# Kernel tuning notes

Hardware: AMD Instinct MI355X
Metric: run time of the kernel (lower is better)

## Reference

```python
import jax, jax.numpy as jnp
import numpy as np

N = 50000   # nodes
E = 800000  # edges (avg degree 16)
D = 96      # input feature dim
U = 96      # units (== D, so no dense_i projection)


def _glorot(key, fan_in, fan_out):
    limit = np.sqrt(6.0 / (fan_in + fan_out)).astype(np.float32)
    return jax.random.uniform(key, (fan_in, fan_out), jnp.float32, -limit, limit)


def setup_inputs() -> dict:
    key = jax.random.key(0)
    ks = jax.random.split(key, 8)
    X = jax.random.normal(ks[0], (N, D), jnp.float32)
    row = jax.random.randint(ks[1], (E,), 0, N, jnp.int32)   # destination nodes
    col = jax.random.randint(ks[2], (E,), 0, N, jnp.int32)   # source nodes
    a_vals = jax.random.uniform(ks[3], (E,), jnp.float32)    # adjacency values
    return {
        "X": X,
        "a_vals": a_vals,
        "Wn": _glorot(ks[4], D, U), "bn": jnp.zeros((U,), jnp.float32),
        "Wgi": _glorot(ks[5], D, U), "bgi": jnp.zeros((U,), jnp.float32),
        "Wgn": _glorot(ks[6], U, U), "bgn": jnp.zeros((U,), jnp.float32),
        "row": row, "col": col,
    }


def reference(X, a_vals, Wn, bn, Wgi, bgi, Wgn, bgn, row, col):
    # new_X = dense_n(X); new_X = A @ new_X  (SpMM via gather + segment_sum)
    newX = X @ Wn + bn                       # [N, U]
    msgs = a_vals[:, None] * newX[col]       # [E, U]
    agg = jax.ops.segment_sum(msgs, row, num_segments=N)  # [N, U]
    # gate = sigmoid(dense_gate_i(X) + dense_gate_n(agg))
    gate = jax.nn.sigmoid(X @ Wgi + bgi + agg @ Wgn + bgn)
    # units == inp_dim -> no dense_i; gated residual combine
    return agg * gate + X * (1.0 - gate)
```

## Files before the change

kernel.cpp:

```cpp
#include <hip/hip_runtime.h>
#include <math.h>


#define DU 96
#define DU4 24
#define NCH 12
#define CAP 32

typedef unsigned int uint;
typedef unsigned short ushort;
typedef __attribute__((ext_vector_type(8))) short short8;
typedef __attribute__((ext_vector_type(4))) float f32x4;

__device__ inline uint bf16r(float x) {
  uint u = __float_as_uint(x);
  return (u + 0x7FFFu + ((u >> 16) & 1u)) >> 16;
}

__global__ __launch_bounds__(256) void k_fuse1(
    const float* __restrict__ X, const float* __restrict__ Wn,
    const float* __restrict__ bn, const float* __restrict__ Wgi,
    const float* __restrict__ Wgn, const int* __restrict__ row,
    const int* __restrict__ col, const float* __restrict__ a_vals,
    ushort* __restrict__ Xb, ushort* __restrict__ newXb,
    ushort* __restrict__ WTgi, ushort* __restrict__ WTgn,
    int* __restrict__ cnt8, int2* __restrict__ epad8, int N, int E, int ntile) {
  __shared__ ushort WL[9216];
  __shared__ ushort Xs[64][104];
  const int tid = threadIdx.x;
  const int lane = tid & 63, w = tid >> 6;
  const int m = lane & 15, q = lane >> 4;

  if ((int)blockIdx.x < ntile) {
    if (blockIdx.x == 0) {
      for (int i = tid; i < DU * DU; i += 256) {
        int n = i / DU, k = i % DU;
        WTgi[i] = (ushort)bf16r(Wgi[k * DU + n]);
      }
    } else if (blockIdx.x == 1) {
      for (int i = tid; i < DU * DU; i += 256) {
        int n = i / DU, k = i % DU;
        WTgn[i] = (ushort)bf16r(Wgn[k * DU + n]);
      }
    }
    for (int idx = tid; idx < 9216; idx += 256) {
      int j = idx & 7, ln = (idx >> 3) & 63, tk = idx >> 9;
      int ks = tk / 6, t = tk % 6;
      int k = ks * 32 + (ln >> 4) * 8 + j;
      int n = t * 16 + (ln & 15);
      WL[idx] = (ushort)bf16r(Wn[k * DU + n]);
    }
    const int row0 = blockIdx.x * 64;
    for (int i = tid; i < 64 * 48; i += 256) {
      int r = i / 48, cu = i % 48;
      int gr = row0 + r;
      uint packed = 0;
      if (gr < N) {
        float2 v = ((const float2*)X)[(size_t)gr * 48 + cu];
        packed = bf16r(v.x) | (bf16r(v.y) << 16);
        ((uint*)Xb)[(size_t)gr * 48 + cu] = packed;
      }
      *(uint*)&Xs[r][cu * 2] = packed;
    }
    __syncthreads();

    f32x4 acc[6];
#pragma unroll
    for (int t = 0; t < 6; ++t) acc[t] = (f32x4){0.f, 0.f, 0.f, 0.f};
#pragma unroll
    for (int ks = 0; ks < 3; ++ks) {
      short8 af = *(const short8*)&Xs[w * 16 + m][ks * 32 + q * 8];
#pragma unroll
      for (int t = 0; t < 6; ++t) {
        short8 bf = *(const short8*)&WL[((ks * 6 + t) * 64 + lane) * 8];
        acc[t] = __builtin_amdgcn_mfma_f32_16x16x32_bf16(af, bf, acc[t], 0, 0, 0);
      }
    }
    __syncthreads();
#pragma unroll
    for (int t = 0; t < 6; ++t) {
      int c = t * 16 + m;
      float bb = bn[c];
#pragma unroll
      for (int i = 0; i < 4; ++i)
        Xs[w * 16 + q * 4 + i][c] = (ushort)bf16r(acc[t][i] + bb);
    }
    __syncthreads();
    for (int i = tid; i < 64 * 48; i += 256) {
      int r = i / 48, cu = i % 48;
      int gr = row0 + r;
      if (gr < N) ((uint*)newXb)[(size_t)gr * 48 + cu] = *(uint*)&Xs[r][cu * 2];
    }
  }

  {
    const int g = blockIdx.x & 7;
    int* cnt = cnt8 + (size_t)g * N;
    int2* ep = epad8 + (size_t)g * N * CAP;
    for (int i = blockIdx.x * 256 + tid; i < E; i += gridDim.x * 256) {
      int d = row[i];
      int slot = atomicAdd(&cnt[d], 1);
      if (slot < CAP)
        ep[(size_t)d * CAP + slot] = make_int2(col[i], __float_as_int(a_vals[i]));
    }
  }
}

__global__ __launch_bounds__(256) void k_agg(const ushort* __restrict__ newXb,
                                             const int* __restrict__ cnt8,
                                             const int2* __restrict__ epad8,
                                             ushort* __restrict__ aggb, int N) {
  int i = blockIdx.x * 256 + threadIdx.x;
  int r = i / NCH;
  int c = i % NCH;
  if (r >= N) return;
  float acc[8];
#pragma unroll
  for (int j = 0; j < 8; ++j) acc[j] = 0.f;

#pragma unroll
  for (int g = 0; g < 8; ++g) {
    int e1 = cnt8[(size_t)g * N + r];
    if (e1 > CAP) e1 = CAP;
    const int2* ep = epad8 + ((size_t)g * N + r) * CAP;
    int e = 0;
    for (; e + 2 <= e1; e += 2) {
      int2 p0 = ep[e + 0];
      int2 p1 = ep[e + 1];
      uint4 v0 = *(const uint4*)(newXb + (size_t)p0.x * DU + c * 8);
      uint4 v1 = *(const uint4*)(newXb + (size_t)p1.x * DU + c * 8);
      float a0 = __int_as_float(p0.y), a1 = __int_as_float(p1.y);
      acc[0] = fmaf(a0, __uint_as_float(v0.x << 16), acc[0]);
      acc[1] = fmaf(a0, __uint_as_float(v0.x & 0xFFFF0000u), acc[1]);
      acc[2] = fmaf(a0, __uint_as_float(v0.y << 16), acc[2]);
      acc[3] = fmaf(a0, __uint_as_float(v0.y & 0xFFFF0000u), acc[3]);
      acc[4] = fmaf(a0, __uint_as_float(v0.z << 16), acc[4]);
      acc[5] = fmaf(a0, __uint_as_float(v0.z & 0xFFFF0000u), acc[5]);
      acc[6] = fmaf(a0, __uint_as_float(v0.w << 16), acc[6]);
      acc[7] = fmaf(a0, __uint_as_float(v0.w & 0xFFFF0000u), acc[7]);
      acc[0] = fmaf(a1, __uint_as_float(v1.x << 16), acc[0]);
      acc[1] = fmaf(a1, __uint_as_float(v1.x & 0xFFFF0000u), acc[1]);
      acc[2] = fmaf(a1, __uint_as_float(v1.y << 16), acc[2]);
      acc[3] = fmaf(a1, __uint_as_float(v1.y & 0xFFFF0000u), acc[3]);
      acc[4] = fmaf(a1, __uint_as_float(v1.z << 16), acc[4]);
      acc[5] = fmaf(a1, __uint_as_float(v1.z & 0xFFFF0000u), acc[5]);
      acc[6] = fmaf(a1, __uint_as_float(v1.w << 16), acc[6]);
      acc[7] = fmaf(a1, __uint_as_float(v1.w & 0xFFFF0000u), acc[7]);
    }
    if (e < e1) {
      int2 p = ep[e];
      uint4 v = *(const uint4*)(newXb + (size_t)p.x * DU + c * 8);
      float a = __int_as_float(p.y);
      acc[0] = fmaf(a, __uint_as_float(v.x << 16), acc[0]);
      acc[1] = fmaf(a, __uint_as_float(v.x & 0xFFFF0000u), acc[1]);
      acc[2] = fmaf(a, __uint_as_float(v.y << 16), acc[2]);
      acc[3] = fmaf(a, __uint_as_float(v.y & 0xFFFF0000u), acc[3]);
      acc[4] = fmaf(a, __uint_as_float(v.z << 16), acc[4]);
      acc[5] = fmaf(a, __uint_as_float(v.z & 0xFFFF0000u), acc[5]);
      acc[6] = fmaf(a, __uint_as_float(v.w << 16), acc[6]);
      acc[7] = fmaf(a, __uint_as_float(v.w & 0xFFFF0000u), acc[7]);
    }
  }
  uint4 o;
  o.x = bf16r(acc[0]) | (bf16r(acc[1]) << 16);
  o.y = bf16r(acc[2]) | (bf16r(acc[3]) << 16);
  o.z = bf16r(acc[4]) | (bf16r(acc[5]) << 16);
  o.w = bf16r(acc[6]) | (bf16r(acc[7]) << 16);
  *(uint4*)(aggb + (size_t)r * DU + c * 8) = o;
}

__global__ __launch_bounds__(256) void k_gateM(const ushort* __restrict__ Xb,
                                               const ushort* __restrict__ aggb,
                                               const ushort* __restrict__ WTgi,
                                               const ushort* __restrict__ WTgn,
                                               const float* __restrict__ bgi,
                                               const float* __restrict__ bgn,
                                               const float* __restrict__ X,
                                               float* __restrict__ Out, int N) {
  __shared__ float Gs[64][100];
  const int tid = threadIdx.x;
  const int lane = tid & 63, w = tid >> 6;
  const int m = lane & 15, q = lane >> 4;
  const int row0 = blockIdx.x * 64;
  int ar = row0 + w * 16 + m;
  if (ar > N - 1) ar = N - 1;

  f32x4 acc[6];
#pragma unroll
  for (int t = 0; t < 6; ++t) acc[t] = (f32x4){0.f, 0.f, 0.f, 0.f};

#pragma unroll
  for (int ks = 0; ks < 3; ++ks) {
    short8 af = *(const short8*)(Xb + (size_t)ar * DU + ks * 32 + q * 8);
#pragma unroll
    for (int t = 0; t < 6; ++t) {
      short8 bf = *(const short8*)(WTgi + (size_t)(t * 16 + m) * DU + ks * 32 + q * 8);
      acc[t] = __builtin_amdgcn_mfma_f32_16x16x32_bf16(af, bf, acc[t], 0, 0, 0);
    }
  }
#pragma unroll
  for (int ks = 0; ks < 3; ++ks) {
    short8 af = *(const short8*)(aggb + (size_t)ar * DU + ks * 32 + q * 8);
#pragma unroll
    for (int t = 0; t < 6; ++t) {
      short8 bf = *(const short8*)(WTgn + (size_t)(t * 16 + m) * DU + ks * 32 + q * 8);
      acc[t] = __builtin_amdgcn_mfma_f32_16x16x32_bf16(af, bf, acc[t], 0, 0, 0);
    }
  }

#pragma unroll
  for (int t = 0; t < 6; ++t) {
    int c = t * 16 + m;
    float bb = bgi[c] + bgn[c];
#pragma unroll
    for (int i = 0; i < 4; ++i) {
      float z = acc[t][i] + bb;
      Gs[w * 16 + q * 4 + i][c] = 1.f / (1.f + __expf(-z));
    }
  }
  __syncthreads();

  for (int j = tid; j < 64 * DU4; j += 256) {
    int r = j / DU4, c = j % DU4;
    int gr = row0 + r;
    if (gr < N) {
      float4 xv = ((const float4*)X)[(size_t)gr * DU4 + c];
      uint2 av = ((const uint2*)aggb)[(size_t)gr * DU4 + c];
      float a0 = __uint_as_float(av.x << 16);
      float a1 = __uint_as_float(av.x & 0xFFFF0000u);
      float a2 = __uint_as_float(av.y << 16);
      float a3 = __uint_as_float(av.y & 0xFFFF0000u);
      const float* gp = &Gs[r][c * 4];
      float4 o;
      o.x = xv.x + gp[0] * (a0 - xv.x);
      o.y = xv.y + gp[1] * (a1 - xv.y);
      o.z = xv.z + gp[2] * (a2 - xv.z);
      o.w = xv.w + gp[3] * (a3 - xv.w);
      ((float4*)Out)[(size_t)gr * DU4 + c] = o;
    }
  }
}

extern "C" void kernel_launch(void* const* d_in, const int* in_sizes, int n_in,
                              void* d_out, int out_size, void* d_ws, size_t ws_size,
                              hipStream_t stream) {
  const float* X      = (const float*)d_in[0];
  const float* a_vals = (const float*)d_in[1];
  const float* Wn     = (const float*)d_in[2];
  const float* bn     = (const float*)d_in[3];
  const float* Wgi    = (const float*)d_in[4];
  const float* bgi    = (const float*)d_in[5];
  const float* Wgn    = (const float*)d_in[6];
  const float* bgn    = (const float*)d_in[7];
  const int*   row    = (const int*)d_in[8];
  const int*   col    = (const int*)d_in[9];
  float* out = (float*)d_out;

  const int N = in_sizes[0] / DU;
  const int E = in_sizes[1];
  const int ntile = (N + 63) / 64;
  const int G1 = ((ntile + 7) / 8) * 8;

  int2*   epad8 = (int2*)d_ws;
  ushort* Xb    = (ushort*)(epad8 + (size_t)8 * N * CAP);
  ushort* newXb = Xb + (size_t)N * DU;
  ushort* aggb  = newXb + (size_t)N * DU;
  ushort* WTgi  = aggb + (size_t)N * DU;
  ushort* WTgn  = WTgi + DU * DU;
  int*    cnt8  = (int*)(WTgn + DU * DU);

  hipMemsetAsync(cnt8, 0, (size_t)8 * N * sizeof(int), stream);

  k_fuse1<<<G1, 256, 0, stream>>>(X, Wn, bn, Wgi, Wgn, row, col, a_vals,
                                  Xb, newXb, WTgi, WTgn, cnt8, epad8, N, E, ntile);
  k_agg  <<<((size_t)N * NCH + 255) / 256, 256, 0, stream>>>(newXb, cnt8, epad8, aggb, N);
  k_gateM<<<ntile, 256, 0, stream>>>(Xb, aggb, WTgi, WTgn, bgi, bgn, X, out, N);
}
```

Before: 224.4 us.

## Fuse SpMM aggregation into gate kernel and interleave per-node edge buckets

Merges the aggregation kernel into the gate/MFMA kernel so aggregated rows stay in shared memory rather than going through a global bf16 buffer, which removes one launch and the aggb write and reread. The edge padding layout changes from eight separate per-group arrays (cap 32 each) to one interleaved 128-slot region per node (cap 16 per group), giving better locality for a node's edges. The fused kernel uses 512 threads and splits the MFMA columns across wave pairs. The risks are less parallelism during the gather phase, since each block only has 768 work items, and dropped edges if a node gets more than 16 edges from one group.

```diff
diff --git a/kernel.cpp b/kernel.cpp
--- a/kernel.cpp
+++ b/kernel.cpp
@@ -4,8 +4,7 @@
 
 #define DU 96
 #define DU4 24
-#define NCH 12
-#define CAP 32
+#define CAPG 16
 
 typedef unsigned int uint;
 typedef unsigned short ushort;
@@ -24,7 +23,7 @@
     const int* __restrict__ col, const float* __restrict__ a_vals,
     ushort* __restrict__ Xb, ushort* __restrict__ newXb,
     ushort* __restrict__ WTgi, ushort* __restrict__ WTgn,
-    int* __restrict__ cnt8, int2* __restrict__ epad8, int N, int E, int ntile) {
+    int* __restrict__ cnt8, int2* __restrict__ epad, int N, int E, int ntile) {
   __shared__ ushort WL[9216];
   __shared__ ushort Xs[64][104];
   const int tid = threadIdx.x;
@@ -96,136 +95,141 @@
   {
     const int g = blockIdx.x & 7;
     int* cnt = cnt8 + (size_t)g * N;
-    int2* ep = epad8 + (size_t)g * N * CAP;
     for (int i = blockIdx.x * 256 + tid; i < E; i += gridDim.x * 256) {
       int d = row[i];
       int slot = atomicAdd(&cnt[d], 1);
-      if (slot < CAP)
-        ep[(size_t)d * CAP + slot] = make_int2(col[i], __float_as_int(a_vals[i]));
-    }
-  }
-}
-
-__global__ __launch_bounds__(256) void k_agg(const ushort* __restrict__ newXb,
-                                             const int* __restrict__ cnt8,
-                                             const int2* __restrict__ epad8,
-                                             ushort* __restrict__ aggb, int N) {
-  int i = blockIdx.x * 256 + threadIdx.x;
-  int r = i / NCH;
-  int c = i % NCH;
-  if (r >= N) return;
-  float acc[8];
-#pragma unroll
-  for (int j = 0; j < 8; ++j) acc[j] = 0.f;
-
-#pragma unroll
-  for (int g = 0; g < 8; ++g) {
-    int e1 = cnt8[(size_t)g * N + r];
-    if (e1 > CAP) e1 = CAP;
-    const int2* ep = epad8 + ((size_t)g * N + r) * CAP;
-    int e = 0;
-    for (; e + 2 <= e1; e += 2) {
-      int2 p0 = ep[e + 0];
-      int2 p1 = ep[e + 1];
-      uint4 v0 = *(const uint4*)(newXb + (size_t)p0.x * DU + c * 8);
-      uint4 v1 = *(const uint4*)(newXb + (size_t)p1.x * DU + c * 8);
-      float a0 = __int_as_float(p0.y), a1 = __int_as_float(p1.y);
-      acc[0] = fmaf(a0, __uint_as_float(v0.x << 16), acc[0]);
-      acc[1] = fmaf(a0, __uint_as_float(v0.x & 0xFFFF0000u), acc[1]);
-      acc[2] = fmaf(a0, __uint_as_float(v0.y << 16), acc[2]);
-      acc[3] = fmaf(a0, __uint_as_float(v0.y & 0xFFFF0000u), acc[3]);
-      acc[4] = fmaf(a0, __uint_as_float(v0.z << 16), acc[4]);
-      acc[5] = fmaf(a0, __uint_as_float(v0.z & 0xFFFF0000u), acc[5]);
-      acc[6] = fmaf(a0, __uint_as_float(v0.w << 16), acc[6]);
-      acc[7] = fmaf(a0, __uint_as_float(v0.w & 0xFFFF0000u), acc[7]);
-      acc[0] = fmaf(a1, __uint_as_float(v1.x << 16), acc[0]);
-      acc[1] = fmaf(a1, __uint_as_float(v1.x & 0xFFFF0000u), acc[1]);
-      acc[2] = fmaf(a1, __uint_as_float(v1.y << 16), acc[2]);
-      acc[3] = fmaf(a1, __uint_as_float(v1.y & 0xFFFF0000u), acc[3]);
-      acc[4] = fmaf(a1, __uint_as_float(v1.z << 16), acc[4]);
-      acc[5] = fmaf(a1, __uint_as_float(v1.z & 0xFFFF0000u), acc[5]);
-      acc[6] = fmaf(a1, __uint_as_float(v1.w << 16), acc[6]);
-      acc[7] = fmaf(a1, __uint_as_float(v1.w & 0xFFFF0000u), acc[7]);
-    }
-    if (e < e1) {
-      int2 p = ep[e];
-      uint4 v = *(const uint4*)(newXb + (size_t)p.x * DU + c * 8);
-      float a = __int_as_float(p.y);
-      acc[0] = fmaf(a, __uint_as_float(v.x << 16), acc[0]);
-      acc[1] = fmaf(a, __uint_as_float(v.x & 0xFFFF0000u), acc[1]);
-      acc[2] = fmaf(a, __uint_as_float(v.y << 16), acc[2]);
-      acc[3] = fmaf(a, __uint_as_float(v.y & 0xFFFF0000u), acc[3]);
-      acc[4] = fmaf(a, __uint_as_float(v.z << 16), acc[4]);
-      acc[5] = fmaf(a, __uint_as_float(v.z & 0xFFFF0000u), acc[5]);
-      acc[6] = fmaf(a, __uint_as_float(v.w << 16), acc[6]);
-      acc[7] = fmaf(a, __uint_as_float(v.w & 0xFFFF0000u), acc[7]);
-    }
-  }
-  uint4 o;
-  o.x = bf16r(acc[0]) | (bf16r(acc[1]) << 16);
-  o.y = bf16r(acc[2]) | (bf16r(acc[3]) << 16);
-  o.z = bf16r(acc[4]) | (bf16r(acc[5]) << 16);
-  o.w = bf16r(acc[6]) | (bf16r(acc[7]) << 16);
-  *(uint4*)(aggb + (size_t)r * DU + c * 8) = o;
-}
-
-__global__ __launch_bounds__(256) void k_gateM(const ushort* __restrict__ Xb,
-                                               const ushort* __restrict__ aggb,
-                                               const ushort* __restrict__ WTgi,
-                                               const ushort* __restrict__ WTgn,
-                                               const float* __restrict__ bgi,
-                                               const float* __restrict__ bgn,
-                                               const float* __restrict__ X,
-                                               float* __restrict__ Out, int N) {
+      if (slot < CAPG)
+        epad[(size_t)d * 128 + g * CAPG + slot] =
+            make_int2(col[i], __float_as_int(a_vals[i]));
+    }
+  }
+}
+
+__global__ __launch_bounds__(512) void k_aggGate(
+    const ushort* __restrict__ Xb, const ushort* __restrict__ newXb,
+    const int* __restrict__ cnt8, const int2* __restrict__ epad,
+    const ushort* __restrict__ WTgi, const ushort* __restrict__ WTgn,
+    const float* __restrict__ bgi, const float* __restrict__ bgn,
+    const float* __restrict__ X, float* __restrict__ Out, int N) {
+  __shared__ ushort As[64][104];
   __shared__ float Gs[64][100];
   const int tid = threadIdx.x;
-  const int lane = tid & 63, w = tid >> 6;
+  const int lane = tid & 63;
   const int m = lane & 15, q = lane >> 4;
   const int row0 = blockIdx.x * 64;
-  int ar = row0 + w * 16 + m;
-  if (ar > N - 1) ar = N - 1;
-
-  f32x4 acc[6];
-#pragma unroll
-  for (int t = 0; t < 6; ++t) acc[t] = (f32x4){0.f, 0.f, 0.f, 0.f};
-
-#pragma unroll
-  for (int ks = 0; ks < 3; ++ks) {
-    short8 af = *(const short8*)(Xb + (size_t)ar * DU + ks * 32 + q * 8);
-#pragma unroll
-    for (int t = 0; t < 6; ++t) {
-      short8 bf = *(const short8*)(WTgi + (size_t)(t * 16 + m) * DU + ks * 32 + q * 8);
-      acc[t] = __builtin_amdgcn_mfma_f32_16x16x32_bf16(af, bf, acc[t], 0, 0, 0);
-    }
-  }
-#pragma unroll
-  for (int ks = 0; ks < 3; ++ks) {
-    short8 af = *(const short8*)(aggb + (size_t)ar * DU + ks * 32 + q * 8);
-#pragma unroll
-    for (int t = 0; t < 6; ++t) {
-      short8 bf = *(const short8*)(WTgn + (size_t)(t * 16 + m) * DU + ks * 32 + q * 8);
-      acc[t] = __builtin_amdgcn_mfma_f32_16x16x32_bf16(af, bf, acc[t], 0, 0, 0);
-    }
-  }
-
-#pragma unroll
-  for (int t = 0; t < 6; ++t) {
-    int c = t * 16 + m;
-    float bb = bgi[c] + bgn[c];
-#pragma unroll
-    for (int i = 0; i < 4; ++i) {
-      float z = acc[t][i] + bb;
-      Gs[w * 16 + q * 4 + i][c] = 1.f / (1.f + __expf(-z));
-    }
+
+  for (int j = tid; j < 64 * 12; j += 512) {
+    int lr = j / 12, c = j % 12;
+    int r = row0 + lr;
+    float acc[8];
+#pragma unroll
+    for (int k = 0; k < 8; ++k) acc[k] = 0.f;
+    if (r < N) {
+      const int2* epr = epad + (size_t)r * 128;
+#pragma unroll
+      for (int g = 0; g < 8; ++g) {
+        int e1 = cnt8[(size_t)g * N + r];
+        if (e1 > CAPG) e1 = CAPG;
+        const int2* ep = epr + g * CAPG;
+        int e = 0;
+        for (; e + 2 <= e1; e += 2) {
+          int2 p0 = ep[e + 0];
+          int2 p1 = ep[e + 1];
+          uint4 v0 = *(const uint4*)(newXb + (size_t)p0.x * DU + c * 8);
+          uint4 v1 = *(const uint4*)(newXb + (size_t)p1.x * DU + c * 8);
+          float a0 = __int_as_float(p0.y), a1 = __int_as_float(p1.y);
+          acc[0] = fmaf(a0, __uint_as_float(v0.x << 16), acc[0]);
+          acc[1] = fmaf(a0, __uint_as_float(v0.x & 0xFFFF0000u), acc[1]);
+          acc[2] = fmaf(a0, __uint_as_float(v0.y << 16), acc[2]);
+          acc[3] = fmaf(a0, __uint_as_float(v0.y & 0xFFFF0000u), acc[3]);
+          acc[4] = fmaf(a0, __uint_as_float(v0.z << 16), acc[4]);
+          acc[5] = fmaf(a0, __uint_as_float(v0.z & 0xFFFF0000u), acc[5]);
+          acc[6] = fmaf(a0, __uint_as_float(v0.w << 16), acc[6]);
+          acc[7] = fmaf(a0, __uint_as_float(v0.w & 0xFFFF0000u), acc[7]);
+          acc[0] = fmaf(a1, __uint_as_float(v1.x << 16), acc[0]);
+          acc[1] = fmaf(a1, __uint_as_float(v1.x & 0xFFFF0000u), acc[1]);
+          acc[2] = fmaf(a1, __uint_as_float(v1.y << 16), acc[2]);
+          acc[3] = fmaf(a1, __uint_as_float(v1.y & 0xFFFF0000u), acc[3]);
+          acc[4] = fmaf(a1, __uint_as_float(v1.z << 16), acc[4]);
+          acc[5] = fmaf(a1, __uint_as_float(v1.z & 0xFFFF0000u), acc[5]);
+          acc[6] = fmaf(a1, __uint_as_float(v1.w << 16), acc[6]);
+          acc[7] = fmaf(a1, __uint_as_float(v1.w & 0xFFFF0000u), acc[7]);
+        }
+        if (e < e1) {
+          int2 p = ep[e];
+          uint4 v = *(const uint4*)(newXb + (size_t)p.x * DU + c * 8);
+          float a = __int_as_float(p.y);
+          acc[0] = fmaf(a, __uint_as_float(v.x << 16), acc[0]);
+          acc[1] = fmaf(a, __uint_as_float(v.x & 0xFFFF0000u), acc[1]);
+          acc[2] = fmaf(a, __uint_as_float(v.y << 16), acc[2]);
+          acc[3] = fmaf(a, __uint_as_float(v.y & 0xFFFF0000u), acc[3]);
+          acc[4] = fmaf(a, __uint_as_float(v.z << 16), acc[4]);
+          acc[5] = fmaf(a, __uint_as_float(v.z & 0xFFFF0000u), acc[5]);
+          acc[6] = fmaf(a, __uint_as_float(v.w << 16), acc[6]);
+          acc[7] = fmaf(a, __uint_as_float(v.w & 0xFFFF0000u), acc[7]);
+        }
+      }
+    }
+    uint4 o;
+    o.x = bf16r(acc[0]) | (bf16r(acc[1]) << 16);
+    o.y = bf16r(acc[2]) | (bf16r(acc[3]) << 16);
+    o.z = bf16r(acc[4]) | (bf16r(acc[5]) << 16);
+    o.w = bf16r(acc[6]) | (bf16r(acc[7]) << 16);
+    *(uint4*)&As[lr][c * 8] = o;
   }
   __syncthreads();
 
-  for (int j = tid; j < 64 * DU4; j += 256) {
+  {
+    const int wv = tid >> 6;
+    const int rg = wv >> 1;
+    const int ch = wv & 1;
+    int ar = row0 + rg * 16 + m;
+    if (ar > N - 1) ar = N - 1;
+    const int lr = rg * 16 + m;
+
+    f32x4 acc[3];
+#pragma unroll
+    for (int t = 0; t < 3; ++t) acc[t] = (f32x4){0.f, 0.f, 0.f, 0.f};
+
+#pragma unroll
+    for (int ks = 0; ks < 3; ++ks) {
+      short8 af = *(const short8*)(Xb + (size_t)ar * DU + ks * 32 + q * 8);
+#pragma unroll
+      for (int tt = 0; tt < 3; ++tt) {
+        int t = ch * 3 + tt;
+        short8 bf = *(const short8*)(WTgi + (size_t)(t * 16 + m) * DU + ks * 32 + q * 8);
+        acc[tt] = __builtin_amdgcn_mfma_f32_16x16x32_bf16(af, bf, acc[tt], 0, 0, 0);
+      }
+    }
+#pragma unroll
+    for (int ks = 0; ks < 3; ++ks) {
+      short8 af = *(const short8*)&As[lr][ks * 32 + q * 8];
+#pragma unroll
+      for (int tt = 0; tt < 3; ++tt) {
+        int t = ch * 3 + tt;
+        short8 bf = *(const short8*)(WTgn + (size_t)(t * 16 + m) * DU + ks * 32 + q * 8);
+        acc[tt] = __builtin_amdgcn_mfma_f32_16x16x32_bf16(af, bf, acc[tt], 0, 0, 0);
+      }
+    }
+#pragma unroll
+    for (int tt = 0; tt < 3; ++tt) {
+      int c = (ch * 3 + tt) * 16 + m;
+      float bb = bgi[c] + bgn[c];
+#pragma unroll
+      for (int i = 0; i < 4; ++i) {
+        float z = acc[tt][i] + bb;
+        Gs[rg * 16 + q * 4 + i][c] = 1.f / (1.f + __expf(-z));
+      }
+    }
+  }
+  __syncthreads();
+
+  for (int j = tid; j < 64 * DU4; j += 512) {
     int r = j / DU4, c = j % DU4;
     int gr = row0 + r;
     if (gr < N) {
       float4 xv = ((const float4*)X)[(size_t)gr * DU4 + c];
-      uint2 av = ((const uint2*)aggb)[(size_t)gr * DU4 + c];
+      uint2 av = *(const uint2*)&As[r][c * 4];
       float a0 = __uint_as_float(av.x << 16);
       float a1 = __uint_as_float(av.x & 0xFFFF0000u);
       float a2 = __uint_as_float(av.y << 16);
@@ -261,18 +265,17 @@
   const int ntile = (N + 63) / 64;
   const int G1 = ((ntile + 7) / 8) * 8;
 
-  int2*   epad8 = (int2*)d_ws;
-  ushort* Xb    = (ushort*)(epad8 + (size_t)8 * N * CAP);
+  int2*   epad  = (int2*)d_ws;
+  ushort* Xb    = (ushort*)(epad + (size_t)N * 128 + 128);
   ushort* newXb = Xb + (size_t)N * DU;
-  ushort* aggb  = newXb + (size_t)N * DU;
-  ushort* WTgi  = aggb + (size_t)N * DU;
+  ushort* WTgi  = newXb + (size_t)N * DU;
   ushort* WTgn  = WTgi + DU * DU;
   int*    cnt8  = (int*)(WTgn + DU * DU);
 
   hipMemsetAsync(cnt8, 0, (size_t)8 * N * sizeof(int), stream);
 
   k_fuse1<<<G1, 256, 0, stream>>>(X, Wn, bn, Wgi, Wgn, row, col, a_vals,
-                                  Xb, newXb, WTgi, WTgn, cnt8, epad8, N, E, ntile);
-  k_agg  <<<((size_t)N * NCH + 255) / 256, 256, 0, stream>>>(newXb, cnt8, epad8, aggb, N);
-  k_gateM<<<ntile, 256, 0, stream>>>(Xb, aggb, WTgi, WTgn, bgi, bgn, X, out, N);
-}
+                                  Xb, newXb, WTgi, WTgn, cnt8, epad, N, E, ntile);
+  k_aggGate<<<ntile, 512, 0, stream>>>(Xb, newXb, cnt8, epad, WTgi, WTgn,
+                                       bgi, bgn, X, out, N);
+}
```

Measured after the change: 220.6 us. No clear change (-1.7%).
